# Optimization experiments

Measured on AMD Instinct MI355X. Metric: run time of the kernel, lower is better.

The kernel has to match this reference:

```python
import jax, jax.numpy as jnp
import numpy as np

Q = 1          # hard-coded in the original forward
LAM = 1e-3     # ridge regularizer of the ELM-AE least-squares solve


def setup_inputs() -> dict:
    key = jax.random.key(0)
    k1, k2 = jax.random.split(key)
    B, Z, H, W = 64, 512, 32, 32
    x = jax.random.normal(k1, (B, Z, H, W), dtype=jnp.float32)
    # fixed random ELM hidden-layer weights (Q x z); the repo generates these
    # with a deterministic LCG, here plain gaussian random
    Wh = jax.random.normal(k2, (Q, Z), dtype=jnp.float32)
    return {"x": x, "W": Wh}


def reference(x, W):
    # x: [B, Z, h, w]  -> per-sample feature matrix X: [Z, N] with N = h*w pixels
    B, Z, h, w = x.shape
    X = x.reshape(B, Z, h * w)                      # [B, Z, N]
    # ELM-AE: random hidden activations over pixels
    Hh = jax.nn.sigmoid(jnp.einsum('qz,bzn->bqn', W, X))   # [B, Q, N]
    G = jnp.einsum('bqn,bpn->bqp', Hh, Hh) + LAM * jnp.eye(Q, dtype=x.dtype)  # [B, Q, Q]
    XHt = jnp.einsum('bzn,bqn->bzq', X, Hh)         # [B, Z, Q]
    # solve G^T Beta^T = XHt^T  (G symmetric)
    Beta = jnp.swapaxes(jnp.linalg.solve(G, jnp.swapaxes(XHt, 1, 2)), 1, 2)  # [B, Z, Q]
    # pooled features flattened to (B, Q*Z, 1) as in the original
    out = Beta.reshape(B, Q * Z, 1)
    return out
```

## Files before the change

kernel.cpp:

```cpp
#include <hip/hip_runtime.h>
#include <hip/hip_bf16.h>

#define B_ 64
#define Z_ 512
#define N_ 1024
#define LAM 1e-3f
#define PB 16
#define NC 64
#define TH 1024
#define WS_XH (B_ * PB * Z_)
#define WS_G  (B_ * PB)

__global__ __launch_bounds__(TH, 8) void elm_k1(
    const float* __restrict__ x, const float* __restrict__ Wh,
    float* __restrict__ pxh, float* __restrict__ gws) {
  __shared__ float part[16][NC];
  __shared__ float h_lds[NC];

  const int t   = threadIdx.x;
  const int blk = blockIdx.x;
  const int b   = blk >> 4;
  const int p   = blk & 15;
  const int jg  = t & 15;
  const int zr  = t >> 4;
  const int wv  = t >> 6;
  const int ln  = t & 63;

  const float* xp = x + (size_t)b * (Z_ * N_) + (size_t)zr * N_ + (p * NC + jg * 4);

  float4 v[8];
#pragma unroll
  for (int k = 0; k < 8; ++k)
    v[k] = *reinterpret_cast<const float4*>(xp + (size_t)(64 * k) * N_);

  float w[8];
#pragma unroll
  for (int k = 0; k < 8; ++k) w[k] = Wh[zr + 64 * k];

  float sp[4];
#pragma unroll
  for (int i = 0; i < 4; ++i) {
    float s = 0.f;
#pragma unroll
    for (int k = 0; k < 8; ++k) s += w[k] * reinterpret_cast<const float*>(&v[k])[i];
    s += __shfl_xor(s, 16);
    s += __shfl_xor(s, 32);
    sp[i] = s;
  }
  if (ln < 16) {
#pragma unroll
    for (int i = 0; i < 4; ++i) part[wv][ln * 4 + i] = sp[i];
  }
  __syncthreads();

  if (t < NC) {
    float s = 0.f;
#pragma unroll
    for (int w16 = 0; w16 < 16; ++w16) s += part[w16][t];
    const float h = 1.f / (1.f + __expf(-s));
    h_lds[t] = h;
    float q = h * h;
    q += __shfl_xor(q, 1);
    q += __shfl_xor(q, 2);
    q += __shfl_xor(q, 4);
    q += __shfl_xor(q, 8);
    q += __shfl_xor(q, 16);
    q += __shfl_xor(q, 32);
    if (t == 0) gws[blk] = q;
  }
  __syncthreads();

  float acc[8] = {0.f, 0.f, 0.f, 0.f, 0.f, 0.f, 0.f, 0.f};
#pragma unroll
  for (int i = 0; i < 4; ++i) {
    const float h = h_lds[jg * 4 + i];
#pragma unroll
    for (int k = 0; k < 8; ++k) acc[k] += h * reinterpret_cast<const float*>(&v[k])[i];
  }
#pragma unroll
  for (int k = 0; k < 8; ++k) {
    float a = acc[k];
    a += __shfl_xor(a, 1);
    a += __shfl_xor(a, 2);
    a += __shfl_xor(a, 4);
    a += __shfl_xor(a, 8);
    if (jg == 0) pxh[(size_t)blk * Z_ + zr + 64 * k] = a;
  }
}

__global__ __launch_bounds__(Z_) void elm_k2(
    const float* __restrict__ pxh, const float* __restrict__ gws,
    float* __restrict__ out) {
  const int b = blockIdx.x;
  const int t = threadIdx.x;
  __shared__ float ginv;
  if (t < PB) {
    float g = gws[b * PB + t];
    g += __shfl_xor(g, 1);
    g += __shfl_xor(g, 2);
    g += __shfl_xor(g, 4);
    g += __shfl_xor(g, 8);
    if (t == 0) ginv = 1.f / (g + LAM);
  }
  __syncthreads();
  float s = 0.f;
#pragma unroll
  for (int p = 0; p < PB; ++p) s += pxh[((size_t)b * PB + p) * Z_ + t];
  out[b * Z_ + t] = s * ginv;
}

extern "C" void kernel_launch(void* const* d_in, const int* in_sizes, int n_in,
                              void* d_out, int out_size, void* d_ws, size_t ws_size,
                              hipStream_t stream) {
  const float* x  = (const float*)d_in[0];
  const float* Wh = (const float*)d_in[1];
  float* out = (float*)d_out;
  float* pxh = (float*)d_ws;
  float* gws = (float*)d_ws + WS_XH;

  elm_k1<<<dim3(B_ * PB), dim3(TH), 0, stream>>>(x, Wh, pxh, gws);
  elm_k2<<<dim3(B_), dim3(Z_), 0, stream>>>(pxh, gws, out);
}
```

Baseline: 29.22 us.

## Fuse reduction kernel into main kernel via atomics and last-block finalization

Replaces the per-block partial writes and the second reduction kernel with global atomicAdd accumulation into per-batch buffers. A per-batch arrival counter lets the last of the 16 blocks for each batch read the totals and write the scaled output. A memset of the accumulators is added before the launch. This swaps one kernel launch and a partial-buffer round trip for a memset, float atomics (nondeterministic summation order), and a last-block pattern that relies on atomic visibility without an explicit fence.

```diff
diff --git a/kernel.cpp b/kernel.cpp
--- a/kernel.cpp
+++ b/kernel.cpp
@@ -8,14 +8,19 @@
 #define PB 16
 #define NC 64
 #define TH 1024
-#define WS_XH (B_ * PB * Z_)
-#define WS_G  (B_ * PB)
+#define WS_ACCXH 0
+#define WS_ACCG  (B_ * Z_)
+#define WS_CNT   (B_ * Z_ + B_)
+#define WS_ZERO_BYTES ((B_ * Z_ + B_ + B_) * 4)
 
 __global__ __launch_bounds__(TH, 8) void elm_k1(
     const float* __restrict__ x, const float* __restrict__ Wh,
-    float* __restrict__ pxh, float* __restrict__ gws) {
+    float* __restrict__ accxh, float* __restrict__ accg,
+    unsigned int* __restrict__ cnt, float* __restrict__ out) {
   __shared__ float part[16][NC];
   __shared__ float h_lds[NC];
+  __shared__ unsigned int tick;
+  __shared__ float ginv;
 
   const int t   = threadIdx.x;
   const int blk = blockIdx.x;
@@ -66,7 +71,7 @@
     q += __shfl_xor(q, 8);
     q += __shfl_xor(q, 16);
     q += __shfl_xor(q, 32);
-    if (t == 0) gws[blk] = q;
+    if (t == 0) atomicAdd(&accg[b], q);
   }
   __syncthreads();
 
@@ -84,29 +89,23 @@
     a += __shfl_xor(a, 2);
     a += __shfl_xor(a, 4);
     a += __shfl_xor(a, 8);
-    if (jg == 0) pxh[(size_t)blk * Z_ + zr + 64 * k] = a;
+    if (jg == 0) atomicAdd(&accxh[b * Z_ + zr + 64 * k], a);
   }
-}
 
-__global__ __launch_bounds__(Z_) void elm_k2(
-    const float* __restrict__ pxh, const float* __restrict__ gws,
-    float* __restrict__ out) {
-  const int b = blockIdx.x;
-  const int t = threadIdx.x;
-  __shared__ float ginv;
-  if (t < PB) {
-    float g = gws[b * PB + t];
-    g += __shfl_xor(g, 1);
-    g += __shfl_xor(g, 2);
-    g += __shfl_xor(g, 4);
-    g += __shfl_xor(g, 8);
-    if (t == 0) ginv = 1.f / (g + LAM);
+  __syncthreads();
+  if (t == 0) tick = atomicAdd(&cnt[b], 1u);
+  __syncthreads();
+  if (tick == PB - 1) {
+    if (t == 0) {
+      const float g = atomicAdd(&accg[b], 0.f);
+      ginv = 1.f / (g + LAM);
+    }
+    __syncthreads();
+    if (t < Z_) {
+      const float s = atomicAdd(&accxh[b * Z_ + t], 0.f);
+      out[b * Z_ + t] = s * ginv;
+    }
   }
-  __syncthreads();
-  float s = 0.f;
-#pragma unroll
-  for (int p = 0; p < PB; ++p) s += pxh[((size_t)b * PB + p) * Z_ + t];
-  out[b * Z_ + t] = s * ginv;
 }
 
 extern "C" void kernel_launch(void* const* d_in, const int* in_sizes, int n_in,
@@ -115,9 +114,10 @@
   const float* x  = (const float*)d_in[0];
   const float* Wh = (const float*)d_in[1];
   float* out = (float*)d_out;
-  float* pxh = (float*)d_ws;
-  float* gws = (float*)d_ws + WS_XH;
+  float* accxh = (float*)d_ws + WS_ACCXH;
+  float* accg  = (float*)d_ws + WS_ACCG;
+  unsigned int* cnt = (unsigned int*)((float*)d_ws + WS_CNT);
 
-  elm_k1<<<dim3(B_ * PB), dim3(TH), 0, stream>>>(x, Wh, pxh, gws);
-  elm_k2<<<dim3(B_), dim3(Z_), 0, stream>>>(pxh, gws, out);
+  hipMemsetAsync(d_ws, 0, WS_ZERO_BYTES, stream);
+  elm_k1<<<dim3(B_ * PB), dim3(TH), 0, stream>>>(x, Wh, accxh, accg, cnt, out);
 }
```

Measured after the change: 37.02 us. +26.7%, slower.
